# Performance work log

Measured on AMD Instinct MI355X. Metric: run time of the kernel, lower is better.

## Reference

```python
import jax, jax.numpy as jnp
import numpy as np

NBINS = 256


def _equalize_hist(img):
    # img: [H, W] float32 with values in [0, 255]; replicates cv2.equalizeHist
    vals = jnp.clip(img.astype(jnp.int32), 0, NBINS - 1).reshape(-1)
    hist = jnp.zeros((NBINS,), jnp.float32).at[vals].add(1.0)
    cdf = jnp.cumsum(hist)
    total = jnp.float32(vals.shape[0])
    # cdf value at the first nonzero bin (cv2 maps that bin to 0)
    cdf_min = cdf[jnp.argmax(hist > 0)]
    scale = (NBINS - 1.0) / jnp.maximum(total - cdf_min, 1.0)
    lut = jnp.clip(jnp.round((cdf - cdf_min) * scale), 0.0, 255.0)
    return lut[vals].reshape(img.shape) / 255.0


def setup_inputs() -> dict:
    key = jax.random.key(0)
    k1, _ = jax.random.split(key)
    # uint8-like pixel values stored as float32, shape [B, 1, H, W]
    image = jnp.floor(jax.random.uniform(k1, (64, 1, 1024, 1024), jnp.float32) * 256.0)
    image = jnp.clip(image, 0.0, 255.0)
    kernel = jnp.array([[[[0.0, 1.0, 0.0], [1.0, -4.0, 1.0], [0.0, 1.0, 0.0]]]], jnp.float32)
    return {"image": image, "kernel": kernel}


def reference(image, kernel):
    # per-image histogram equalization (channels == 1, as in the torch loop)
    eq = jax.vmap(_equalize_hist)(image[:, 0, :, :])[:, None, :, :]  # [B,1,H,W]
    laplace = jax.lax.conv_general_dilated(
        eq, kernel,
        window_strides=(1, 1), padding=((1, 1), (1, 1)),
        dimension_numbers=("NCHW", "OIHW", "NCHW"))
    # torch.var defaults to unbiased (ddof=1) over all elements
    return jnp.var(laplace, ddof=1)
```

## Files before the change

### kernel.cpp

```cpp
#include <hip/hip_runtime.h>

#define W 1024
#define H 1024
#define NIMG 64
#define NBINS 256
#define NPIX (W * H)
#define NTOT ((long long)NIMG * NPIX)
#define HBLK 64
#define RPW 16
#define LGRIDX (H / (RPW * 4))

typedef float f32x4 __attribute__((ext_vector_type(4)));

#define WS_PART 0
#define WS_LUT  (4u * 1024 * 1024)
#define WS_ACC  (WS_LUT + 64 * 1024)
#define WS_U8   (8u * 1024 * 1024)

__global__ __launch_bounds__(256) void hist_kernel(const float* __restrict__ img,
                                                   unsigned int* __restrict__ part,
                                                   unsigned char* __restrict__ u8img) {
    __shared__ unsigned int lh[NBINS];
    const int b = blockIdx.y;
    lh[threadIdx.x] = 0u;
    __syncthreads();
    const size_t base = (size_t)b * NPIX;
    const f32x4* p = (const f32x4*)(img + base);
    uchar4* q8 = (uchar4*)(u8img + base);
    const int nvec = NPIX / 4;
    const int stride = gridDim.x * 256;
    for (int i = blockIdx.x * 256 + threadIdx.x; i < nvec; i += stride) {
        f32x4 v = __builtin_nontemporal_load(&p[i]);
        int i0 = min(max((int)v[0], 0), 255);
        int i1 = min(max((int)v[1], 0), 255);
        int i2 = min(max((int)v[2], 0), 255);
        int i3 = min(max((int)v[3], 0), 255);
        atomicAdd(&lh[i0], 1u);
        atomicAdd(&lh[i1], 1u);
        atomicAdd(&lh[i2], 1u);
        atomicAdd(&lh[i3], 1u);
        q8[i] = make_uchar4((unsigned char)i0, (unsigned char)i1,
                            (unsigned char)i2, (unsigned char)i3);
    }
    __syncthreads();
    part[((size_t)b * HBLK + blockIdx.x) * NBINS + threadIdx.x] = lh[threadIdx.x];
}

__global__ __launch_bounds__(256) void lut_kernel(const unsigned int* __restrict__ part,
                                                  unsigned int* __restrict__ lut32) {
    __shared__ float cdf[NBINS];
    __shared__ float s_min;
    const int b = blockIdx.x;
    const int t = threadIdx.x;
    unsigned int h = 0;
#pragma unroll 8
    for (int blk = 0; blk < HBLK; ++blk)
        h += part[((size_t)b * HBLK + blk) * NBINS + t];
    cdf[t] = (float)h;
    __syncthreads();
    for (int off = 1; off < NBINS; off <<= 1) {
        float add = (t >= off) ? cdf[t - off] : 0.0f;
        __syncthreads();
        cdf[t] += add;
        __syncthreads();
    }
    if (t == 0) {
        float m = 0.0f;
        for (int i = 0; i < NBINS; ++i) {
            if (cdf[i] > 0.0f) { m = cdf[i]; break; }
        }
        s_min = m;
    }
    __syncthreads();
    const float scale = 255.0f / fmaxf((float)NPIX - s_min, 1.0f);
    float L = fminf(fmaxf(rintf((cdf[t] - s_min) * scale), 0.0f), 255.0f);
    lut32[b * NBINS + t] = (unsigned int)L;
}

__global__ __launch_bounds__(256) void lap_kernel(const unsigned char* __restrict__ u8img,
                                                  const unsigned int* __restrict__ lut32,
                                                  unsigned long long* __restrict__ acc) {
    __shared__ unsigned int slut[NBINS];
    const int b = blockIdx.y;
    slut[threadIdx.x] = lut32[b * NBINS + threadIdx.x];
    __syncthreads();

    const int lane = threadIdx.x & 63;
    const int wv = threadIdx.x >> 6;
    const int y0 = blockIdx.x * (RPW * 4) + wv * RPW;
    const unsigned char* rowp = u8img + (size_t)b * NPIX + lane * 16;

    int pr[16], cr[16], nr[16];

    auto load_raw = [&](int gy, uint4& raw) {
        if ((unsigned)gy < (unsigned)H) raw = *(const uint4*)(rowp + (size_t)gy * W);
        else raw = make_uint4(0u, 0u, 0u, 0u);
    };
    auto gather = [&](const uint4& raw, bool valid, int out[16]) {
        const unsigned int w[4] = {raw.x, raw.y, raw.z, raw.w};
        if (valid) {
#pragma unroll
            for (int k = 0; k < 4; ++k)
#pragma unroll
                for (int j = 0; j < 4; ++j)
                    out[4 * k + j] = (int)slut[(w[k] >> (8 * j)) & 0xFFu];
        } else {
#pragma unroll
            for (int p = 0; p < 16; ++p) out[p] = 0;
        }
    };

    uint4 rawC, rawN;
    load_raw(y0 - 1, rawC);
    gather(rawC, y0 - 1 >= 0, pr);
    load_raw(y0, rawC);
    gather(rawC, true, cr);
    load_raw(y0 + 1, rawC);

    int s = 0, q = 0;
#pragma unroll
    for (int rr = 0; rr < RPW; ++rr) {
        const int gy = y0 + rr;
        load_raw(gy + 2, rawN);
        gather(rawC, gy + 1 < H, nr);

        int lw = __shfl_up(cr[15], 1, 64);
        lw = (lane == 0) ? 0 : lw;
        int rw = __shfl_down(cr[0], 1, 64);
        rw = (lane == 63) ? 0 : rw;

#pragma unroll
        for (int p = 0; p < 16; ++p) {
            const int l = (p == 0) ? lw : cr[p - 1];
            const int r = (p == 15) ? rw : cr[p + 1];
            const int lap = pr[p] + nr[p] + l + r - 4 * cr[p];
            s += lap;
            q += lap * lap;
        }
#pragma unroll
        for (int p = 0; p < 16; ++p) { pr[p] = cr[p]; cr[p] = nr[p]; }
        rawC = rawN;
    }

    long long S = s, Q = q;
    for (int off = 32; off > 0; off >>= 1) {
        S += __shfl_down(S, off, 64);
        Q += __shfl_down(Q, off, 64);
    }
    __shared__ long long ss[4], sq[4];
    if (lane == 0) { ss[wv] = S; sq[wv] = Q; }
    __syncthreads();
    if (threadIdx.x == 0) {
        long long St = ss[0] + ss[1] + ss[2] + ss[3];
        long long Qt = sq[0] + sq[1] + sq[2] + sq[3];
        const int blk = blockIdx.x + blockIdx.y * gridDim.x;
        acc[2 * blk]     = (unsigned long long)St;
        acc[2 * blk + 1] = (unsigned long long)Qt;
    }
}

__global__ __launch_bounds__(256) void finalize_kernel(const unsigned long long* __restrict__ acc,
                                                       float* __restrict__ out) {
    const int t = threadIdx.x;
    long long S = 0, Q = 0;
#pragma unroll
    for (int i = 0; i < NIMG * LGRIDX; i += 256) {
        S += (long long)acc[2 * (i + t)];
        Q += (long long)acc[2 * (i + t) + 1];
    }
    for (int off = 32; off > 0; off >>= 1) {
        S += __shfl_down(S, off, 64);
        Q += __shfl_down(Q, off, 64);
    }
    __shared__ long long ss[4], sq[4];
    const int wave = t >> 6, lane = t & 63;
    if (lane == 0) { ss[wave] = S; sq[wave] = Q; }
    __syncthreads();
    if (t == 0) {
        long long St = ss[0] + ss[1] + ss[2] + ss[3];
        long long Qt = sq[0] + sq[1] + sq[2] + sq[3];
        const double N = (double)NTOT;
        double Sr = (double)St / 255.0;
        double Qr = (double)Qt / 65025.0;
        out[0] = (float)((Qr - Sr * Sr / N) / (N - 1.0));
    }
}

extern "C" void kernel_launch(void* const* d_in, const int* in_sizes, int n_in,
                              void* d_out, int out_size, void* d_ws, size_t ws_size,
                              hipStream_t stream) {
    const float* img = (const float*)d_in[0];
    float* out = (float*)d_out;

    unsigned int* part      = (unsigned int*)((char*)d_ws + WS_PART);
    unsigned int* lut32     = (unsigned int*)((char*)d_ws + WS_LUT);
    unsigned long long* acc = (unsigned long long*)((char*)d_ws + WS_ACC);
    unsigned char* u8img    = (unsigned char*)((char*)d_ws + WS_U8);

    dim3 hgrid(HBLK, NIMG);
    hist_kernel<<<hgrid, 256, 0, stream>>>(img, part, u8img);

    lut_kernel<<<NIMG, NBINS, 0, stream>>>(part, lut32);

    dim3 lgrid(LGRIDX, NIMG);
    lap_kernel<<<lgrid, 256, 0, stream>>>(u8img, lut32, acc);

    finalize_kernel<<<1, 256, 0, stream>>>(acc, out);
}
```

Baseline: 129.2 us.

## Fuse LUT build and finalize into Laplacian kernel with last-block reduction

Removes the separate LUT and finalize launches: each Laplacian block now rebuilds its image's LUT from the partial histograms, and the final variance is computed by the last block via atomic accumulation and a ticket counter. Control counters are zeroed inside the histogram kernel. This cuts launch and inter-kernel gaps at the cost of redundant histogram reduction and scan in every block, plus global atomics.

```diff
diff --git a/kernel.cpp b/kernel.cpp
--- a/kernel.cpp
+++ b/kernel.cpp
@@ -9,19 +9,21 @@
 #define HBLK 64
 #define RPW 16
 #define LGRIDX (H / (RPW * 4))
+#define NBLK (LGRIDX * NIMG)
 
 typedef float f32x4 __attribute__((ext_vector_type(4)));
 
 #define WS_PART 0
-#define WS_LUT  (4u * 1024 * 1024)
-#define WS_ACC  (WS_LUT + 64 * 1024)
+#define WS_CTRL (4u * 1024 * 1024)
 #define WS_U8   (8u * 1024 * 1024)
 
 __global__ __launch_bounds__(256) void hist_kernel(const float* __restrict__ img,
                                                    unsigned int* __restrict__ part,
-                                                   unsigned char* __restrict__ u8img) {
+                                                   unsigned char* __restrict__ u8img,
+                                                   unsigned long long* __restrict__ ctrl) {
     __shared__ unsigned int lh[NBINS];
     const int b = blockIdx.y;
+    if (blockIdx.x == 0 && b == 0 && threadIdx.x < 3) ctrl[threadIdx.x] = 0ULL;
     lh[threadIdx.x] = 0u;
     __syncthreads();
     const size_t base = (size_t)b * NPIX;
@@ -46,12 +48,16 @@
     part[((size_t)b * HBLK + blockIdx.x) * NBINS + threadIdx.x] = lh[threadIdx.x];
 }
 
-__global__ __launch_bounds__(256) void lut_kernel(const unsigned int* __restrict__ part,
-                                                  unsigned int* __restrict__ lut32) {
+__global__ __launch_bounds__(256) void lap_kernel(const unsigned char* __restrict__ u8img,
+                                                  const unsigned int* __restrict__ part,
+                                                  unsigned long long* __restrict__ ctrl,
+                                                  float* __restrict__ out) {
     __shared__ float cdf[NBINS];
+    __shared__ unsigned int slut[NBINS];
     __shared__ float s_min;
-    const int b = blockIdx.x;
+    const int b = blockIdx.y;
     const int t = threadIdx.x;
+
     unsigned int h = 0;
 #pragma unroll 8
     for (int blk = 0; blk < HBLK; ++blk)
@@ -64,29 +70,14 @@
         cdf[t] += add;
         __syncthreads();
     }
-    if (t == 0) {
-        float m = 0.0f;
-        for (int i = 0; i < NBINS; ++i) {
-            if (cdf[i] > 0.0f) { m = cdf[i]; break; }
-        }
-        s_min = m;
-    }
+    if (cdf[t] > 0.0f && (t == 0 || cdf[t - 1] == 0.0f)) s_min = cdf[t];
     __syncthreads();
     const float scale = 255.0f / fmaxf((float)NPIX - s_min, 1.0f);
-    float L = fminf(fmaxf(rintf((cdf[t] - s_min) * scale), 0.0f), 255.0f);
-    lut32[b * NBINS + t] = (unsigned int)L;
-}
-
-__global__ __launch_bounds__(256) void lap_kernel(const unsigned char* __restrict__ u8img,
-                                                  const unsigned int* __restrict__ lut32,
-                                                  unsigned long long* __restrict__ acc) {
-    __shared__ unsigned int slut[NBINS];
-    const int b = blockIdx.y;
-    slut[threadIdx.x] = lut32[b * NBINS + threadIdx.x];
+    slut[t] = (unsigned int)fminf(fmaxf(rintf((cdf[t] - s_min) * scale), 0.0f), 255.0f);
     __syncthreads();
 
-    const int lane = threadIdx.x & 63;
-    const int wv = threadIdx.x >> 6;
+    const int lane = t & 63;
+    const int wv = t >> 6;
     const int y0 = blockIdx.x * (RPW * 4) + wv * RPW;
     const unsigned char* rowp = u8img + (size_t)b * NPIX + lane * 16;
 
@@ -96,17 +87,17 @@
         if ((unsigned)gy < (unsigned)H) raw = *(const uint4*)(rowp + (size_t)gy * W);
         else raw = make_uint4(0u, 0u, 0u, 0u);
     };
-    auto gather = [&](const uint4& raw, bool valid, int out[16]) {
+    auto gather = [&](const uint4& raw, bool valid, int outp[16]) {
         const unsigned int w[4] = {raw.x, raw.y, raw.z, raw.w};
         if (valid) {
 #pragma unroll
             for (int k = 0; k < 4; ++k)
 #pragma unroll
                 for (int j = 0; j < 4; ++j)
-                    out[4 * k + j] = (int)slut[(w[k] >> (8 * j)) & 0xFFu];
+                    outp[4 * k + j] = (int)slut[(w[k] >> (8 * j)) & 0xFFu];
         } else {
 #pragma unroll
-            for (int p = 0; p < 16; ++p) out[p] = 0;
+            for (int p = 0; p < 16; ++p) outp[p] = 0;
         }
     };
 
@@ -150,39 +141,22 @@
     __shared__ long long ss[4], sq[4];
     if (lane == 0) { ss[wv] = S; sq[wv] = Q; }
     __syncthreads();
-    if (threadIdx.x == 0) {
-        long long St = ss[0] + ss[1] + ss[2] + ss[3];
-        long long Qt = sq[0] + sq[1] + sq[2] + sq[3];
-        const int blk = blockIdx.x + blockIdx.y * gridDim.x;
-        acc[2 * blk]     = (unsigned long long)St;
-        acc[2 * blk + 1] = (unsigned long long)Qt;
-    }
-}
-
-__global__ __launch_bounds__(256) void finalize_kernel(const unsigned long long* __restrict__ acc,
-                                                       float* __restrict__ out) {
-    const int t = threadIdx.x;
-    long long S = 0, Q = 0;
-#pragma unroll
-    for (int i = 0; i < NIMG * LGRIDX; i += 256) {
-        S += (long long)acc[2 * (i + t)];
-        Q += (long long)acc[2 * (i + t) + 1];
-    }
-    for (int off = 32; off > 0; off >>= 1) {
-        S += __shfl_down(S, off, 64);
-        Q += __shfl_down(Q, off, 64);
-    }
-    __shared__ long long ss[4], sq[4];
-    const int wave = t >> 6, lane = t & 63;
-    if (lane == 0) { ss[wave] = S; sq[wave] = Q; }
-    __syncthreads();
     if (t == 0) {
         long long St = ss[0] + ss[1] + ss[2] + ss[3];
         long long Qt = sq[0] + sq[1] + sq[2] + sq[3];
-        const double N = (double)NTOT;
-        double Sr = (double)St / 255.0;
-        double Qr = (double)Qt / 65025.0;
-        out[0] = (float)((Qr - Sr * Sr / N) / (N - 1.0));
+        atomicAdd(&ctrl[0], (unsigned long long)St);
+        atomicAdd(&ctrl[1], (unsigned long long)Qt);
+        __threadfence();
+        unsigned long long ticket = atomicAdd(&ctrl[2], 1ULL);
+        if (ticket == (unsigned long long)(NBLK - 1)) {
+            __threadfence();
+            long long Sa = (long long)atomicAdd(&ctrl[0], 0ULL);
+            long long Qa = (long long)atomicAdd(&ctrl[1], 0ULL);
+            const double N = (double)NTOT;
+            double Sr = (double)Sa / 255.0;
+            double Qr = (double)Qa / 65025.0;
+            out[0] = (float)((Qr - Sr * Sr / N) / (N - 1.0));
+        }
     }
 }
 
@@ -192,18 +166,13 @@
     const float* img = (const float*)d_in[0];
     float* out = (float*)d_out;
 
-    unsigned int* part      = (unsigned int*)((char*)d_ws + WS_PART);
-    unsigned int* lut32     = (unsigned int*)((char*)d_ws + WS_LUT);
-    unsigned long long* acc = (unsigned long long*)((char*)d_ws + WS_ACC);
-    unsigned char* u8img    = (unsigned char*)((char*)d_ws + WS_U8);
+    unsigned int* part       = (unsigned int*)((char*)d_ws + WS_PART);
+    unsigned long long* ctrl = (unsigned long long*)((char*)d_ws + WS_CTRL);
+    unsigned char* u8img     = (unsigned char*)((char*)d_ws + WS_U8);
 
     dim3 hgrid(HBLK, NIMG);
-    hist_kernel<<<hgrid, 256, 0, stream>>>(img, part, u8img);
-
-    lut_kernel<<<NIMG, NBINS, 0, stream>>>(part, lut32);
+    hist_kernel<<<hgrid, 256, 0, stream>>>(img, part, u8img, ctrl);
 
     dim3 lgrid(LGRIDX, NIMG);
-    lap_kernel<<<lgrid, 256, 0, stream>>>(u8img, lut32, acc);
-
-    finalize_kernel<<<1, 256, 0, stream>>>(acc, out);
+    lap_kernel<<<lgrid, 256, 0, stream>>>(u8img, part, ctrl, out);
 }
```

After: 156.4 us. 1.21x slower.
